# Performance work log

Measured on AMD Instinct MI355X. Metric: run time of the kernel, lower is better.

## Reference

```python
import jax, jax.numpy as jnp
import numpy as np

DIST_THRESH = 0.1
W_DIST = 0.05
W_CHAMFER = 0.05
W_SEP = 0.0005


def setup_inputs() -> dict:
    key = jax.random.key(0)
    k1, k2, k3, k4 = jax.random.split(key, 4)
    B, N, K = 4, 200000, 64
    return {
        "landmarks_C": jax.random.uniform(k1, (B, N, 3), jnp.float32),          # predicted point coords
        "landmarks_F": jax.random.normal(k2, (B, N, 4), jnp.float32) * 0.05,    # [dist, dx, dy, dz]
        "targets_C": jax.random.uniform(k3, (B, K, 3), jnp.float32),            # GT landmark coords
        "targets_F": jax.random.randint(k4, (B, K), 0, 8),                      # GT landmark class labels
        "classes": jnp.arange(6),                                               # classes to supervise
    }


def reference(landmarks_C, landmarks_F, targets_C, targets_F, classes):
    def per_batch(C_i, F_i, tC, tF):
        # class mask over GT landmarks (replaces boolean indexing in torch)
        mask_k = jnp.any(tF[None, :] == classes[:, None], axis=0)          # [K]
        n_valid = mask_k.sum()
        dists_i = F_i[:, 0]                                                # predicted distance, [N]
        coords_i = C_i + F_i[:, 1:]                                        # refined coords, [N,3]
        # pairwise dists GT landmarks -> raw point coords, invalid classes pushed to +inf
        pd = jnp.linalg.norm(C_i[None, :, :] - tC[:, None, :], axis=-1)    # [K,N]
        pd = jnp.where(mask_k[:, None], pd, jnp.inf)
        min_d = pd.min(axis=0)                                             # [N]
        pm = min_d < DIST_THRESH                                           # points near some GT landmark
        # smooth-L1 (beta=1, sum) on predicted distance; clip(inf)=2*thresh reproduces empty-target fallback
        tgt = jnp.clip(min_d, 0.0, 2.0 * DIST_THRESH)
        diff = dists_i - tgt
        ad = jnp.abs(diff)
        dist_loss = jnp.where(ad < 1.0, 0.5 * diff * diff, ad - 0.5).sum()
        # pairwise dists GT landmarks -> refined coords
        ld = jnp.linalg.norm(coords_i[None, :, :] - tC[:, None, :], axis=-1)  # [K,N]
        ld_m = jnp.where(mask_k[:, None], ld, jnp.inf)
        p2g = jnp.where(pm, ld_m.min(axis=0), 0.0)                         # pred->gt, masked points only
        g2p = jnp.where(mask_k, ld_m.min(axis=1), 0.0)                     # gt->pred, valid GT only
        chamfer = (p2g * p2g).sum() + (g2p * g2p).sum()
        # separation: ratio of dists to 2 nearest (valid) GT landmarks, per masked point
        _, idx = jax.lax.top_k(-pd.T, 2)                                   # [N,2] indices of 2 smallest
        d01 = jnp.take_along_axis(ld.T, idx, axis=1)                       # [N,2]
        sep = jnp.where(pm, d01[:, 0] / d01[:, 1], 0.0).sum()
        sep = jnp.where(n_valid >= 2, sep, 0.0)
        return W_DIST * dist_loss + W_CHAMFER * chamfer + W_SEP * sep

    losses = jax.vmap(per_batch)(landmarks_C, landmarks_F, targets_C, targets_F)
    return losses.mean()
```

## Files before the change

### kernel.cpp

```cpp
#include <hip/hip_runtime.h>


constexpr int KT = 64;
constexpr int P  = 4;
constexpr float DIST_THRESH = 0.1f;
constexpr float W_DIST    = 0.05f;
constexpr float W_CHAMFER = 0.05f;
constexpr float W_SEP     = 0.0005f;
constexpr float PT_SENT = -1e18f;
constexpr float TG_SENT = -1e18f;
constexpr float BIGF  = 3.0e38f;
constexpr float WBIAS = 16.0f;

__device__ __forceinline__ unsigned umin_(unsigned a, unsigned b) { return a < b ? a : b; }
__device__ __forceinline__ unsigned umax_(unsigned a, unsigned b) { return a > b ? a : b; }

__global__ __launch_bounds__(256, 4)
void landmark_fused(const float* __restrict__ C, const float* __restrict__ F,
                    const float* __restrict__ tC, const int* __restrict__ tF,
                    const int* __restrict__ classes, int n_classes,
                    int B, int N, int bpb, int cpb,
                    unsigned int* __restrict__ g2p_ws, float* __restrict__ sums,
                    unsigned int* __restrict__ ticket, float* __restrict__ out)
{
    __shared__ float4 tgt2[2 * KT];
    __shared__ float gredw[4][KT];
    __shared__ float rs[3][4];
    __shared__ int is_last;
    __shared__ float lossb[4];

    const int tid  = threadIdx.x;
    const int lane = tid & 63;
    const int wib  = tid >> 6;
    const int b    = blockIdx.x / bpb;
    const int waves_per_batch = bpb * 4;
    const int wid  = (blockIdx.x - b * bpb) * 4 + wib;

    if (tid < KT) {
        int f = tF[b * KT + tid];
        bool valid = false;
        for (int c = 0; c < n_classes; ++c) valid = valid || (f == classes[c]);
        float x = TG_SENT, y = TG_SENT, z = TG_SENT;
        if (valid) {
            x = tC[(b * KT + tid) * 3 + 0];
            y = tC[(b * KT + tid) * 3 + 1];
            z = tC[(b * KT + tid) * 3 + 2];
        }
        float4 v = make_float4(-2.f * x, -2.f * y, -2.f * z,
                               x * x + y * y + z * z + WBIAS);
        tgt2[tid] = v;
        tgt2[tid + KT] = v;
    }
    __syncthreads();

    const float*  Cb = C + (size_t)b * N * 3;
    const float4* Fb = (const float4*)(F + (size_t)b * N * 4);

    float gmin = BIGF;
    float dist_acc = 0.f, p2g_acc = 0.f, sep_acc = 0.f;

    for (int chunk = wid; chunk < cpb; chunk += waves_per_batch) {
        const int base = chunk * (64 * P);

        float px[P], py[P], pz[P], ppm[P], cx[P], cy[P], cz[P], ccm[P], f0[P];
        bool  vp[P];
        #pragma unroll
        for (int p = 0; p < P; ++p) {
            int n = base + p * 64 + lane;
            bool v = (n < N);
            vp[p] = v;
            int ni = v ? n : 0;
            float4 f4 = Fb[ni];
            float X = Cb[3 * ni + 0], Y = Cb[3 * ni + 1], Z = Cb[3 * ni + 2];
            f0[p] = f4.x;
            if (!v) { X = PT_SENT; Y = PT_SENT; Z = PT_SENT; f4.y = f4.z = f4.w = 0.f; }
            px[p] = X;          py[p] = Y;          pz[p] = Z;
            cx[p] = X + f4.y;   cy[p] = Y + f4.z;   cz[p] = Z + f4.w;
            ppm[p] = fmaf(pz[p], pz[p], fmaf(py[p], py[p], px[p] * px[p])) - WBIAS;
            ccm[p] = fmaf(cz[p], cz[p], fmaf(cy[p], cy[p], cx[p] * cx[p])) - WBIAS;
        }

        unsigned k1[P], k2[P];
        float lmin[P];
        #pragma unroll
        for (int p = 0; p < P; ++p) { k1[p] = 0xFFFFFFFFu; k2[p] = 0xFFFFFFFFu; lmin[p] = BIGF; }

        #pragma unroll 8
        for (int i = 0; i < 64; ++i) {
            const float4 T = tgt2[lane + i];
            const unsigned kk = (unsigned)((lane + i) & 63);
            float dl = BIGF;
            #pragma unroll
            for (int p = 0; p < P; ++p) {
                float keyf = fmaf(px[p], T.x, fmaf(py[p], T.y, fmaf(pz[p], T.z, T.w)));
                float ld2  = fmaf(cx[p], T.x, fmaf(cy[p], T.y, fmaf(cz[p], T.z, T.w)));
                unsigned key = (__float_as_uint(keyf) & 0xFFFFFFC0u) | kk;
                unsigned hi = umax_(k1[p], key);
                k1[p] = umin_(k1[p], key);
                k2[p] = umin_(k2[p], hi);
                lmin[p] = fminf(lmin[p], ld2);
                dl = fminf(dl, ld2 + ccm[p]);
            }
            float got = __shfl(dl, (lane - i) & 63, 64);
            gmin = fminf(gmin, got);
        }

        #pragma unroll
        for (int p = 0; p < P; ++p) {
            float keyf1 = __uint_as_float(k1[p] & 0xFFFFFFC0u);
            float mind = sqrtf(fmaxf(keyf1 + ppm[p], 0.f));
            bool pm = (mind < DIST_THRESH) && vp[p];
            float tgtv = fminf(mind, 2.0f * DIST_THRESH);
            float diff = f0[p] - tgtv;
            float ad = fabsf(diff);
            float sl1 = (ad < 1.0f) ? 0.5f * diff * diff : (ad - 0.5f);
            if (vp[p]) dist_acc += sl1;
            if (pm) {
                p2g_acc += fmaxf(lmin[p] + ccm[p], 0.f);
                int i1 = (int)(k1[p] & 63u), i2 = (int)(k2[p] & 63u);
                float4 T1 = tgt2[i1], T2 = tgt2[i2];
                float l1sq = fmaf(cx[p], T1.x, fmaf(cy[p], T1.y, fmaf(cz[p], T1.z, T1.w))) + ccm[p];
                float l2sq = fmaf(cx[p], T2.x, fmaf(cy[p], T2.y, fmaf(cz[p], T2.z, T2.w))) + ccm[p];
                sep_acc += sqrtf(fmaxf(l1sq, 0.f) / fmaxf(l2sq, 1e-30f));
            }
        }
    }

    float v0 = dist_acc, v1 = p2g_acc, v2 = sep_acc;
    #pragma unroll
    for (int o = 32; o > 0; o >>= 1) {
        v0 += __shfl_down(v0, o, 64);
        v1 += __shfl_down(v1, o, 64);
        v2 += __shfl_down(v2, o, 64);
    }
    if (lane == 0) { rs[0][wib] = v0; rs[1][wib] = v1; rs[2][wib] = v2; }
    gredw[wib][lane] = gmin;
    __syncthreads();

    if (tid < 3) {
        float s = rs[tid][0] + rs[tid][1] + rs[tid][2] + rs[tid][3];
        atomicAdd(&sums[tid * B + b], s);
    }
    if (tid < KT) {
        float g = fminf(fminf(gredw[0][tid], gredw[1][tid]),
                        fminf(gredw[2][tid], gredw[3][tid]));
        g = fmaxf(g, 0.f);
        atomicMax(&g2p_ws[b * KT + tid], ~__float_as_uint(g));
    }

    if (tid == 0) {
        __threadfence();
        unsigned int t = atomicAdd(ticket, 1u);
        is_last = (t == (unsigned int)(gridDim.x - 1));
    }
    __syncthreads();
    if (!is_last) return;

    {
        const int fb = tid >> 6, fk = tid & 63;
        float g = 0.f, nv = 0.f;
        if (fb < B) {
            int f = tF[fb * KT + fk];
            bool valid = false;
            for (int c = 0; c < n_classes; ++c) valid = valid || (f == classes[c]);
            if (valid) {
                nv = 1.f;
                unsigned int enc = atomicMax(&g2p_ws[fb * KT + fk], 0u);
                g = __uint_as_float(~enc);
            }
        }
        #pragma unroll
        for (int o = 32; o > 0; o >>= 1) {
            g  += __shfl_down(g, o, 64);
            nv += __shfl_down(nv, o, 64);
        }
        if (fb < B && fk == 0) {
            float sd = atomicAdd(&sums[0 * B + fb], 0.f);
            float sp = atomicAdd(&sums[1 * B + fb], 0.f);
            float ss = atomicAdd(&sums[2 * B + fb], 0.f);
            float sep = (nv >= 2.f) ? ss : 0.f;
            lossb[fb] = W_DIST * sd + W_CHAMFER * (sp + g) + W_SEP * sep;
        }
        __syncthreads();
        if (tid == 0) {
            float s = 0.f;
            for (int i = 0; i < B; ++i) s += lossb[i];
            out[0] = s / (float)B;
        }
    }
}

extern "C" void kernel_launch(void* const* d_in, const int* in_sizes, int n_in,
                              void* d_out, int out_size, void* d_ws, size_t ws_size,
                              hipStream_t stream)
{
    const float* C       = (const float*)d_in[0];
    const float* F       = (const float*)d_in[1];
    const float* tC      = (const float*)d_in[2];
    const int*   tF      = (const int*)d_in[3];
    const int*   classes = (const int*)d_in[4];
    const int n_classes = in_sizes[4];
    const int B = 4;
    const int N = in_sizes[0] / (3 * B);

    unsigned int* g2p_ws = (unsigned int*)d_ws;
    float*        sums   = (float*)((char*)d_ws + KT * B * 4);
    unsigned int* ticket = (unsigned int*)((char*)d_ws + KT * B * 4 + 12 * 4);

    hipMemsetAsync(d_ws, 0, KT * B * 4 + 16 * 4, stream);

    const int cpb = (N + 64 * P - 1) / (64 * P);
    const int bpb = (cpb + 3) / 4;
    landmark_fused<<<bpb * B, 256, 0, stream>>>(C, F, tC, tF, classes, n_classes,
                                                B, N, bpb, cpb, g2p_ws, sums, ticket,
                                                (float*)d_out);
}
```

Measured before the change: 107.1 us.

## Switch to persistent grid with atomic per-batch chunk work stealing

Replaces the static one-chunk-per-wave grid (about 782 blocks) with a fixed 1024-block persistent grid where each wave grabs chunks from a per-batch atomic counter, with blocks assigned to batches by blockIdx mod 4. Each block now covers many chunks, so the per-block setup and the g2p/sum atomics are paid less often relative to work, and load balance improves. It also restructures the per-iteration g2p min into a tree of fmins. The cost is one atomic per wave per chunk and a B=4 hardcode.

```diff
diff --git a/kernel.cpp b/kernel.cpp
--- a/kernel.cpp
+++ b/kernel.cpp
@@ -19,9 +19,10 @@
 void landmark_fused(const float* __restrict__ C, const float* __restrict__ F,
                     const float* __restrict__ tC, const int* __restrict__ tF,
                     const int* __restrict__ classes, int n_classes,
-                    int B, int N, int bpb, int cpb,
+                    int B, int N, int cpb,
                     unsigned int* __restrict__ g2p_ws, float* __restrict__ sums,
-                    unsigned int* __restrict__ ticket, float* __restrict__ out)
+                    unsigned int* __restrict__ done_ctr,
+                    unsigned int* __restrict__ chunk_tick, float* __restrict__ out)
 {
     __shared__ float4 tgt2[2 * KT];
     __shared__ float gredw[4][KT];
@@ -32,9 +33,7 @@
     const int tid  = threadIdx.x;
     const int lane = tid & 63;
     const int wib  = tid >> 6;
-    const int b    = blockIdx.x / bpb;
-    const int waves_per_batch = bpb * 4;
-    const int wid  = (blockIdx.x - b * bpb) * 4 + wib;
+    const int b    = blockIdx.x & 3;
 
     if (tid < KT) {
         int f = tF[b * KT + tid];
@@ -59,8 +58,12 @@
     float gmin = BIGF;
     float dist_acc = 0.f, p2g_acc = 0.f, sep_acc = 0.f;
 
-    for (int chunk = wid; chunk < cpb; chunk += waves_per_batch) {
-        const int base = chunk * (64 * P);
+    for (;;) {
+        unsigned cgrab = 0;
+        if (lane == 0) cgrab = atomicAdd(&chunk_tick[b], 1u);
+        cgrab = (unsigned)__shfl((int)cgrab, 0, 64);
+        if (cgrab >= (unsigned)cpb) break;
+        const int base = (int)cgrab * (64 * P);
 
         float px[P], py[P], pz[P], ppm[P], cx[P], cy[P], cz[P], ccm[P], f0[P];
         bool  vp[P];
@@ -89,7 +92,7 @@
         for (int i = 0; i < 64; ++i) {
             const float4 T = tgt2[lane + i];
             const unsigned kk = (unsigned)((lane + i) & 63);
-            float dl = BIGF;
+            float a[P];
             #pragma unroll
             for (int p = 0; p < P; ++p) {
                 float keyf = fmaf(px[p], T.x, fmaf(py[p], T.y, fmaf(pz[p], T.z, T.w)));
@@ -99,8 +102,9 @@
                 k1[p] = umin_(k1[p], key);
                 k2[p] = umin_(k2[p], hi);
                 lmin[p] = fminf(lmin[p], ld2);
-                dl = fminf(dl, ld2 + ccm[p]);
+                a[p] = ld2 + ccm[p];
             }
+            float dl = fminf(fminf(a[0], a[1]), fminf(a[2], a[3]));
             float got = __shfl(dl, (lane - i) & 63, 64);
             gmin = fminf(gmin, got);
         }
@@ -139,7 +143,7 @@
 
     if (tid < 3) {
         float s = rs[tid][0] + rs[tid][1] + rs[tid][2] + rs[tid][3];
-        atomicAdd(&sums[tid * B + b], s);
+        atomicAdd(&sums[tid * 4 + b], s);
     }
     if (tid < KT) {
         float g = fminf(fminf(gredw[0][tid], gredw[1][tid]),
@@ -150,7 +154,7 @@
 
     if (tid == 0) {
         __threadfence();
-        unsigned int t = atomicAdd(ticket, 1u);
+        unsigned int t = atomicAdd(done_ctr, 1u);
         is_last = (t == (unsigned int)(gridDim.x - 1));
     }
     __syncthreads();
@@ -159,7 +163,7 @@
     {
         const int fb = tid >> 6, fk = tid & 63;
         float g = 0.f, nv = 0.f;
-        if (fb < B) {
+        if (fb < 4) {
             int f = tF[fb * KT + fk];
             bool valid = false;
             for (int c = 0; c < n_classes; ++c) valid = valid || (f == classes[c]);
@@ -174,18 +178,18 @@
             g  += __shfl_down(g, o, 64);
             nv += __shfl_down(nv, o, 64);
         }
-        if (fb < B && fk == 0) {
-            float sd = atomicAdd(&sums[0 * B + fb], 0.f);
-            float sp = atomicAdd(&sums[1 * B + fb], 0.f);
-            float ss = atomicAdd(&sums[2 * B + fb], 0.f);
+        if (fb < 4 && fk == 0) {
+            float sd = atomicAdd(&sums[0 * 4 + fb], 0.f);
+            float sp = atomicAdd(&sums[1 * 4 + fb], 0.f);
+            float ss = atomicAdd(&sums[2 * 4 + fb], 0.f);
             float sep = (nv >= 2.f) ? ss : 0.f;
             lossb[fb] = W_DIST * sd + W_CHAMFER * (sp + g) + W_SEP * sep;
         }
         __syncthreads();
         if (tid == 0) {
             float s = 0.f;
-            for (int i = 0; i < B; ++i) s += lossb[i];
-            out[0] = s / (float)B;
+            for (int i = 0; i < 4; ++i) s += lossb[i];
+            out[0] = s / 4.0f;
         }
     }
 }
@@ -203,15 +207,15 @@
     const int B = 4;
     const int N = in_sizes[0] / (3 * B);
 
-    unsigned int* g2p_ws = (unsigned int*)d_ws;
-    float*        sums   = (float*)((char*)d_ws + KT * B * 4);
-    unsigned int* ticket = (unsigned int*)((char*)d_ws + KT * B * 4 + 12 * 4);
-
-    hipMemsetAsync(d_ws, 0, KT * B * 4 + 16 * 4, stream);
+    unsigned int* g2p_ws     = (unsigned int*)d_ws;
+    float*        sums       = (float*)((char*)d_ws + 1024);
+    unsigned int* done_ctr   = (unsigned int*)((char*)d_ws + 1072);
+    unsigned int* chunk_tick = (unsigned int*)((char*)d_ws + 1088);
+
+    hipMemsetAsync(d_ws, 0, 2048, stream);
 
     const int cpb = (N + 64 * P - 1) / (64 * P);
-    const int bpb = (cpb + 3) / 4;
-    landmark_fused<<<bpb * B, 256, 0, stream>>>(C, F, tC, tF, classes, n_classes,
-                                                B, N, bpb, cpb, g2p_ws, sums, ticket,
-                                                (float*)d_out);
+    landmark_fused<<<1024, 256, 0, stream>>>(C, F, tC, tF, classes, n_classes,
+                                             B, N, cpb, g2p_ws, sums, done_ctr,
+                                             chunk_tick, (float*)d_out);
 }
```

Measured after the change: 180.3 us. +68.4%, slower.
